# Kernel tuning notes

Hardware: AMD Instinct MI355X
Metric: run time of the kernel (lower is better)

The kernel has to match this reference:

```python
import jax, jax.numpy as jnp
import numpy as np

TEMPERATURE = 8.0  # sqrt(d_k) with d_k = 64


def setup_inputs() -> dict:
    key = jax.random.key(0)
    ks = jax.random.split(key, 5)
    shape = (64, 1024, 64)  # [B*H, N, d_k]
    return {
        "q": jax.random.normal(ks[0], shape, dtype=jnp.float32),
        "k": jax.random.normal(ks[1], shape, dtype=jnp.float32),
        "v": jax.random.normal(ks[2], shape, dtype=jnp.float32),
        "q_sem": jax.random.normal(ks[3], shape, dtype=jnp.float32),
        "k_sem": jax.random.normal(ks[4], shape, dtype=jnp.float32),
    }


def reference(q, k, v, q_sem, k_sem):
    # Semantic fusion branch (q_sem is not None): scores are recomputed
    # with the fused queries/keys. (The original also computes an unused
    # softmax over the pre-fusion scores and an unused attn_sem bmm --
    # dead code with no effect on outputs, so omitted.)
    qf = q + q_sem
    kf = k + k_sem
    attn_score = jnp.einsum("bnd,bmd->bnm", qf, kf) / TEMPERATURE  # [BH, N, N]
    attn = jax.nn.softmax(attn_score, axis=2)
    # dropout in eval mode == identity
    output = jnp.einsum("bnm,bmd->bnd", attn, v)  # [BH, N, d_k]
    return (output, attn, attn_score)
```

## Files before the change

### kernel.cpp

```cpp
#include <hip/hip_runtime.h>
#include <math.h>


#define BH 64
#define N 1024
#define D 64
#define TK 64
#define NC (N / TK)
#define KSTR 68
#define SSTR 68
#define LOG2E 1.44269504088896f
#define ESHIFT (-17.3123404907f)

typedef float    f32x4 __attribute__((ext_vector_type(4)));
typedef _Float16 half8 __attribute__((ext_vector_type(8)));
typedef _Float16 half4 __attribute__((ext_vector_type(4)));
typedef __fp16   fp16x2 __attribute__((ext_vector_type(2)));

__global__ __launch_bounds__(512, 2) void attn_fused_kernel(
    const float* __restrict__ q, const float* __restrict__ k,
    const float* __restrict__ v, const float* __restrict__ qs,
    const float* __restrict__ ks, float* __restrict__ out_o,
    float* __restrict__ out_a, float* __restrict__ out_s)
{
    __shared__ __align__(16) _Float16 Kb[TK][KSTR];
    __shared__ __align__(16) _Float16 Vt[D][KSTR];
    __shared__ __align__(16) float    Sst[32][SSTR];
    __shared__ float rsumf[32];

    const int t  = threadIdx.x;
    const int w  = t >> 6;
    const int l  = t & 63;
    const int lr = l & 15;
    const int lg = l >> 4;
    const int qt = w >> 2;
    const int kt = w & 3;

    const int wg = blockIdx.x;
    const int b  = ((wg >> 8) << 3) | (wg & 7);
    const int q0 = ((wg >> 3) & 31) * 32;

    const size_t inb = (size_t)b * (N * D);
    const size_t sb  = (size_t)b * N * N + (size_t)q0 * N;

    half8 qa[2];
    {
        const float* qp  = q  + inb + (size_t)(q0 + qt * 16 + lr) * D + lg * 8;
        const float* qsp = qs + inb + (size_t)(q0 + qt * 16 + lr) * D + lg * 8;
#pragma unroll
        for (int kst = 0; kst < 2; ++kst) {
            f32x4 a0 = *(const f32x4*)(qp + kst * 32);
            f32x4 a1 = *(const f32x4*)(qp + kst * 32 + 4);
            f32x4 c0 = *(const f32x4*)(qsp + kst * 32);
            f32x4 c1 = *(const f32x4*)(qsp + kst * 32 + 4);
            f32x4 s0 = a0 + c0, s1 = a1 + c1;
            union { half8 h8; fp16x2 h2[4]; } u;
            u.h2[0] = __builtin_amdgcn_cvt_pkrtz(s0[0], s0[1]);
            u.h2[1] = __builtin_amdgcn_cvt_pkrtz(s0[2], s0[3]);
            u.h2[2] = __builtin_amdgcn_cvt_pkrtz(s1[0], s1[1]);
            u.h2[3] = __builtin_amdgcn_cvt_pkrtz(s1[2], s1[3]);
            qa[kst] = u.h8;
        }
    }

    const int  ts = t & 255;
    const bool kstager = (w < 4);
    f32x4 kreg[4], sreg[4], vreg[4];

    auto LOAD = [&](int kc) {
        if (kstager) {
            const f32x4* kbp = (const f32x4*)(k  + inb + (size_t)kc * TK * D);
            const f32x4* sbp = (const f32x4*)(ks + inb + (size_t)kc * TK * D);
#pragma unroll
            for (int j = 0; j < 4; ++j) {
                kreg[j] = kbp[j * 256 + ts];
                sreg[j] = sbp[j * 256 + ts];
            }
        } else {
            const f32x4* vbp = (const f32x4*)(v + inb + (size_t)kc * TK * D);
#pragma unroll
            for (int j = 0; j < 4; ++j)
                vreg[j] = vbp[((ts >> 4) * 4 + j) * 16 + (ts & 15)];
        }
    };
    auto STORE = [&]() {
        if (kstager) {
#pragma unroll
            for (int j = 0; j < 4; ++j) {
                const int row = j * 16 + (ts >> 4), col = (ts & 15) * 4;
                f32x4 sm = kreg[j] + sreg[j];
                union { half4 h4; fp16x2 h2[2]; } u;
                u.h2[0] = __builtin_amdgcn_cvt_pkrtz(sm[0], sm[1]);
                u.h2[1] = __builtin_amdgcn_cvt_pkrtz(sm[2], sm[3]);
                *(half4*)&Kb[row][col] = u.h4;
            }
        } else {
            const int br4 = (ts >> 4) * 4, bc4 = (ts & 15) * 4;
#pragma unroll
            for (int c = 0; c < 4; ++c) {
                union { half4 h4; fp16x2 h2[2]; } u;
                u.h2[0] = __builtin_amdgcn_cvt_pkrtz(vreg[0][c], vreg[1][c]);
                u.h2[1] = __builtin_amdgcn_cvt_pkrtz(vreg[2][c], vreg[3][c]);
                *(half4*)&Vt[bc4 + c][br4] = u.h4;
            }
        }
    };

    LOAD(0);
    STORE();
    LOAD(1);
    __syncthreads();

    f32x4 oacc = {0.f, 0.f, 0.f, 0.f};
    float rs = 0.0f;

    for (int kc = 0; kc < NC; ++kc) {
        {
            half8 kb0 = *(const half8*)&Kb[kt * 16 + lr][lg * 8];
            half8 kb1 = *(const half8*)&Kb[kt * 16 + lr][32 + lg * 8];
            f32x4 ac = {0.f, 0.f, 0.f, 0.f};
            ac = __builtin_amdgcn_mfma_f32_16x16x32_f16(qa[0], kb0, ac, 0, 0, 0);
            ac = __builtin_amdgcn_mfma_f32_16x16x32_f16(qa[1], kb1, ac, 0, 0, 0);
#pragma unroll
            for (int r = 0; r < 4; ++r)
                Sst[qt * 16 + lg * 4 + r][kt * 16 + lr] = ac[r] * 0.125f;
        }
        __syncthreads();

        {
            f32x4 sv = *(const f32x4*)&Sst[t >> 4][(t & 15) * 4];
            *(f32x4*)(out_s + sb + (size_t)(t >> 4) * N + kc * TK + (t & 15) * 4) = sv;
        }

#pragma unroll
        for (int kst = 0; kst < 2; ++kst) {
            f32x4 s0 = *(const f32x4*)&Sst[qt * 16 + lr][kst * 32 + lg * 8];
            f32x4 s1 = *(const f32x4*)&Sst[qt * 16 + lr][kst * 32 + lg * 8 + 4];
            float e[8];
#pragma unroll
            for (int i = 0; i < 4; ++i) {
                e[i]     = __builtin_amdgcn_exp2f(__builtin_fmaf(s0[i], LOG2E, ESHIFT));
                e[i + 4] = __builtin_amdgcn_exp2f(__builtin_fmaf(s1[i], LOG2E, ESHIFT));
            }
            if (kt == 0)
                rs += ((e[0] + e[1]) + (e[2] + e[3])) + ((e[4] + e[5]) + (e[6] + e[7]));
            union { half8 h8; fp16x2 h2[4]; } u;
            u.h2[0] = __builtin_amdgcn_cvt_pkrtz(e[0], e[1]);
            u.h2[1] = __builtin_amdgcn_cvt_pkrtz(e[2], e[3]);
            u.h2[2] = __builtin_amdgcn_cvt_pkrtz(e[4], e[5]);
            u.h2[3] = __builtin_amdgcn_cvt_pkrtz(e[6], e[7]);
            half8 vb = *(const half8*)&Vt[kt * 16 + lr][kst * 32 + lg * 8];
            oacc = __builtin_amdgcn_mfma_f32_16x16x32_f16(u.h8, vb, oacc, 0, 0, 0);
        }

        if (kc + 1 < NC) {
            __syncthreads();
            STORE();
            if (kc + 2 < NC) LOAD(kc + 2);
            __syncthreads();
        }
    }

    if (kt == 0) {
        rs += __shfl_xor(rs, 16);
        rs += __shfl_xor(rs, 32);
        if (l < 16) rsumf[qt * 16 + l] = rs;
    }
    __syncthreads();
    if (t < 32) rsumf[t] = 1.0f / rsumf[t];
    __syncthreads();

#pragma unroll
    for (int r = 0; r < 4; ++r)
        Sst[qt * 16 + lg * 4 + r][kt * 16 + lr] =
            oacc[r] * rsumf[qt * 16 + lg * 4 + r];
    __syncthreads();
    {
        f32x4 ov = *(const f32x4*)&Sst[t >> 4][(t & 15) * 4];
        __builtin_nontemporal_store(ov,
            (f32x4*)(out_o + inb + (size_t)(q0 + (t >> 4)) * D + (t & 15) * 4));
    }

    {
        const int   arow = t >> 4;
        const int   ac0  = (t & 15) * 4;
        const float iva  = rsumf[arow];
        const float* sp  = out_s + sb + (size_t)arow * N + ac0;
        float*       ap  = out_a + sb + (size_t)arow * N + ac0;
#pragma unroll 4
        for (int cb = 0; cb < NC; ++cb) {
            f32x4 sv = *(const f32x4*)(sp + cb * TK);
            f32x4 av;
#pragma unroll
            for (int i = 0; i < 4; ++i)
                av[i] = __builtin_amdgcn_exp2f(__builtin_fmaf(sv[i], LOG2E, ESHIFT)) * iva;
            __builtin_nontemporal_store(av, (f32x4*)(ap + cb * TK));
        }
    }
}

extern "C" void kernel_launch(void* const* d_in, const int* in_sizes, int n_in,
                              void* d_out, int out_size, void* d_ws, size_t ws_size,
                              hipStream_t stream) {
    const float* q  = (const float*)d_in[0];
    const float* k  = (const float*)d_in[1];
    const float* v  = (const float*)d_in[2];
    const float* qs = (const float*)d_in[3];
    const float* ks = (const float*)d_in[4];

    float* out_o = (float*)d_out;
    float* out_a = out_o + (size_t)BH * N * D;
    float* out_s = out_a + (size_t)BH * N * N;

    attn_fused_kernel<<<dim3(BH * (N / 32)), dim3(512), 0, stream>>>(
        q, k, v, qs, ks, out_o, out_a, out_s);
}
```

Baseline: 769.3 us.

## Double-buffer K/V shared tiles and cut per-iteration barriers

Kb and Vt become double-buffered, so the next chunk's store into shared memory can happen right after the QK MFMA instead of in a separate phase. This cuts the loop from three barriers per iteration to two. The barriers are lightweight custom ones (lgkmcnt wait plus s_barrier, wrapped in sched_barriers), which skip waiting on outstanding global loads. Launch bounds request 4 blocks per CU instead of 2. That doubles the per-block shared-memory footprint, and the tighter register budget may cause spills or limit the gain from overlap.

```diff
diff --git a/kernel.cpp b/kernel.cpp
--- a/kernel.cpp
+++ b/kernel.cpp
@@ -12,19 +12,25 @@
 #define LOG2E 1.44269504088896f
 #define ESHIFT (-17.3123404907f)
 
+#define LGKM_BAR() do {                                              \
+    __builtin_amdgcn_sched_barrier(0);                               \
+    asm volatile("s_waitcnt lgkmcnt(0)\n\ts_barrier" ::: "memory");  \
+    __builtin_amdgcn_sched_barrier(0);                               \
+} while (0)
+
 typedef float    f32x4 __attribute__((ext_vector_type(4)));
 typedef _Float16 half8 __attribute__((ext_vector_type(8)));
 typedef _Float16 half4 __attribute__((ext_vector_type(4)));
 typedef __fp16   fp16x2 __attribute__((ext_vector_type(2)));
 
-__global__ __launch_bounds__(512, 2) void attn_fused_kernel(
+__global__ __launch_bounds__(512, 4) void attn_fused_kernel(
     const float* __restrict__ q, const float* __restrict__ k,
     const float* __restrict__ v, const float* __restrict__ qs,
     const float* __restrict__ ks, float* __restrict__ out_o,
     float* __restrict__ out_a, float* __restrict__ out_s)
 {
-    __shared__ __align__(16) _Float16 Kb[TK][KSTR];
-    __shared__ __align__(16) _Float16 Vt[D][KSTR];
+    __shared__ __align__(16) _Float16 Kb[2][TK][KSTR];
+    __shared__ __align__(16) _Float16 Vt[2][D][KSTR];
     __shared__ __align__(16) float    Sst[32][SSTR];
     __shared__ float rsumf[32];
 
@@ -83,7 +89,7 @@
                 vreg[j] = vbp[((ts >> 4) * 4 + j) * 16 + (ts & 15)];
         }
     };
-    auto STORE = [&]() {
+    auto STORE = [&](int bf) {
         if (kstager) {
 #pragma unroll
             for (int j = 0; j < 4; ++j) {
@@ -92,7 +98,7 @@
                 union { half4 h4; fp16x2 h2[2]; } u;
                 u.h2[0] = __builtin_amdgcn_cvt_pkrtz(sm[0], sm[1]);
                 u.h2[1] = __builtin_amdgcn_cvt_pkrtz(sm[2], sm[3]);
-                *(half4*)&Kb[row][col] = u.h4;
+                *(half4*)&Kb[bf][row][col] = u.h4;
             }
         } else {
             const int br4 = (ts >> 4) * 4, bc4 = (ts & 15) * 4;
@@ -101,13 +107,13 @@
                 union { half4 h4; fp16x2 h2[2]; } u;
                 u.h2[0] = __builtin_amdgcn_cvt_pkrtz(vreg[0][c], vreg[1][c]);
                 u.h2[1] = __builtin_amdgcn_cvt_pkrtz(vreg[2][c], vreg[3][c]);
-                *(half4*)&Vt[bc4 + c][br4] = u.h4;
+                *(half4*)&Vt[bf][bc4 + c][br4] = u.h4;
             }
         }
     };
 
     LOAD(0);
-    STORE();
+    STORE(0);
     LOAD(1);
     __syncthreads();
 
@@ -115,9 +121,11 @@
     float rs = 0.0f;
 
     for (int kc = 0; kc < NC; ++kc) {
+        const int c = kc & 1;
+
         {
-            half8 kb0 = *(const half8*)&Kb[kt * 16 + lr][lg * 8];
-            half8 kb1 = *(const half8*)&Kb[kt * 16 + lr][32 + lg * 8];
+            half8 kb0 = *(const half8*)&Kb[c][kt * 16 + lr][lg * 8];
+            half8 kb1 = *(const half8*)&Kb[c][kt * 16 + lr][32 + lg * 8];
             f32x4 ac = {0.f, 0.f, 0.f, 0.f};
             ac = __builtin_amdgcn_mfma_f32_16x16x32_f16(qa[0], kb0, ac, 0, 0, 0);
             ac = __builtin_amdgcn_mfma_f32_16x16x32_f16(qa[1], kb1, ac, 0, 0, 0);
@@ -125,7 +133,11 @@
             for (int r = 0; r < 4; ++r)
                 Sst[qt * 16 + lg * 4 + r][kt * 16 + lr] = ac[r] * 0.125f;
         }
-        __syncthreads();
+
+        if (kc + 1 < NC) STORE(c ^ 1);
+        if (kc + 2 < NC) LOAD(kc + 2);
+
+        LGKM_BAR();
 
         {
             f32x4 sv = *(const f32x4*)&Sst[t >> 4][(t & 15) * 4];
@@ -149,16 +161,11 @@
             u.h2[1] = __builtin_amdgcn_cvt_pkrtz(e[2], e[3]);
             u.h2[2] = __builtin_amdgcn_cvt_pkrtz(e[4], e[5]);
             u.h2[3] = __builtin_amdgcn_cvt_pkrtz(e[6], e[7]);
-            half8 vb = *(const half8*)&Vt[kt * 16 + lr][kst * 32 + lg * 8];
+            half8 vb = *(const half8*)&Vt[c][kt * 16 + lr][kst * 32 + lg * 8];
             oacc = __builtin_amdgcn_mfma_f32_16x16x32_f16(u.h8, vb, oacc, 0, 0, 0);
         }
 
-        if (kc + 1 < NC) {
-            __syncthreads();
-            STORE();
-            if (kc + 2 < NC) LOAD(kc + 2);
-            __syncthreads();
-        }
+        LGKM_BAR();
     }
 
     if (kt == 0) {
```

Measured after the change: 756.5 us. Within noise of the previous version (-1.7%).

## Drop register prefetch of K/V tiles and raise occupancy to four blocks

Applied to the files above, without the earlier changes.

Removes the software-pipelined register prefetch of the next K/K_sem/V chunk and instead loads, converts and stores each chunk into LDS at the top of every iteration. The launch bound goes from 2 to 4 blocks per CU to cut register pressure and let more resident waves hide global-load latency. In exchange, each iteration now waits on its own global loads inside a barrier-bracketed stage with no overlap within a block. Shared memory use per block (about 26 KB) may also limit how many blocks can actually be resident.

```diff
diff --git a/kernel.cpp b/kernel.cpp
--- a/kernel.cpp
+++ b/kernel.cpp
@@ -17,7 +17,7 @@
 typedef _Float16 half4 __attribute__((ext_vector_type(4)));
 typedef __fp16   fp16x2 __attribute__((ext_vector_type(2)));
 
-__global__ __launch_bounds__(512, 2) void attn_fused_kernel(
+__global__ __launch_bounds__(512, 4) void attn_fused_kernel(
     const float* __restrict__ q, const float* __restrict__ k,
     const float* __restrict__ v, const float* __restrict__ qs,
     const float* __restrict__ ks, float* __restrict__ out_o,
@@ -65,56 +65,53 @@
 
     const int  ts = t & 255;
     const bool kstager = (w < 4);
-    f32x4 kreg[4], sreg[4], vreg[4];
-
-    auto LOAD = [&](int kc) {
+
+    auto STAGE = [&](int kc) {
         if (kstager) {
             const f32x4* kbp = (const f32x4*)(k  + inb + (size_t)kc * TK * D);
             const f32x4* sbp = (const f32x4*)(ks + inb + (size_t)kc * TK * D);
 #pragma unroll
-            for (int j = 0; j < 4; ++j) {
-                kreg[j] = kbp[j * 256 + ts];
-                sreg[j] = sbp[j * 256 + ts];
+            for (int h = 0; h < 2; ++h) {
+                f32x4 k0 = kbp[(2 * h)     * 256 + ts];
+                f32x4 k1 = kbp[(2 * h + 1) * 256 + ts];
+                f32x4 s0 = sbp[(2 * h)     * 256 + ts];
+                f32x4 s1 = sbp[(2 * h + 1) * 256 + ts];
+                f32x4 m0 = k0 + s0, m1 = k1 + s1;
+                const int row0 = (2 * h) * 16 + (ts >> 4);
+                const int col  = (ts & 15) * 4;
+                union { half4 h4; fp16x2 h2[2]; } u0, u1;
+                u0.h2[0] = __builtin_amdgcn_cvt_pkrtz(m0[0], m0[1]);
+                u0.h2[1] = __builtin_amdgcn_cvt_pkrtz(m0[2], m0[3]);
+                u1.h2[0] = __builtin_amdgcn_cvt_pkrtz(m1[0], m1[1]);
+                u1.h2[1] = __builtin_amdgcn_cvt_pkrtz(m1[2], m1[3]);
+                *(half4*)&Kb[row0][col]      = u0.h4;
+                *(half4*)&Kb[row0 + 16][col] = u1.h4;
             }
         } else {
             const f32x4* vbp = (const f32x4*)(v + inb + (size_t)kc * TK * D);
-#pragma unroll
-            for (int j = 0; j < 4; ++j)
-                vreg[j] = vbp[((ts >> 4) * 4 + j) * 16 + (ts & 15)];
-        }
-    };
-    auto STORE = [&]() {
-        if (kstager) {
-#pragma unroll
-            for (int j = 0; j < 4; ++j) {
-                const int row = j * 16 + (ts >> 4), col = (ts & 15) * 4;
-                f32x4 sm = kreg[j] + sreg[j];
-                union { half4 h4; fp16x2 h2[2]; } u;
-                u.h2[0] = __builtin_amdgcn_cvt_pkrtz(sm[0], sm[1]);
-                u.h2[1] = __builtin_amdgcn_cvt_pkrtz(sm[2], sm[3]);
-                *(half4*)&Kb[row][col] = u.h4;
-            }
-        } else {
+            f32x4 vr0 = vbp[((ts >> 4) * 4 + 0) * 16 + (ts & 15)];
+            f32x4 vr1 = vbp[((ts >> 4) * 4 + 1) * 16 + (ts & 15)];
+            f32x4 vr2 = vbp[((ts >> 4) * 4 + 2) * 16 + (ts & 15)];
+            f32x4 vr3 = vbp[((ts >> 4) * 4 + 3) * 16 + (ts & 15)];
             const int br4 = (ts >> 4) * 4, bc4 = (ts & 15) * 4;
 #pragma unroll
             for (int c = 0; c < 4; ++c) {
                 union { half4 h4; fp16x2 h2[2]; } u;
-                u.h2[0] = __builtin_amdgcn_cvt_pkrtz(vreg[0][c], vreg[1][c]);
-                u.h2[1] = __builtin_amdgcn_cvt_pkrtz(vreg[2][c], vreg[3][c]);
+                u.h2[0] = __builtin_amdgcn_cvt_pkrtz(vr0[c], vr1[c]);
+                u.h2[1] = __builtin_amdgcn_cvt_pkrtz(vr2[c], vr3[c]);
                 *(half4*)&Vt[bc4 + c][br4] = u.h4;
             }
         }
     };
 
-    LOAD(0);
-    STORE();
-    LOAD(1);
-    __syncthreads();
-
     f32x4 oacc = {0.f, 0.f, 0.f, 0.f};
     float rs = 0.0f;
 
     for (int kc = 0; kc < NC; ++kc) {
+        __syncthreads();
+        STAGE(kc);
+        __syncthreads();
+
         {
             half8 kb0 = *(const half8*)&Kb[kt * 16 + lr][lg * 8];
             half8 kb1 = *(const half8*)&Kb[kt * 16 + lr][32 + lg * 8];
@@ -152,13 +149,6 @@
             half8 vb = *(const half8*)&Vt[kt * 16 + lr][kst * 32 + lg * 8];
             oacc = __builtin_amdgcn_mfma_f32_16x16x32_f16(u.h8, vb, oacc, 0, 0, 0);
         }
-
-        if (kc + 1 < NC) {
-            __syncthreads();
-            STORE();
-            if (kc + 2 < NC) LOAD(kc + 2);
-            __syncthreads();
-        }
     }
 
     if (kt == 0) {
```

Measured after the change: 718.6 us. 6.6% less time.
